# Kernel tuning notes

Hardware: AMD Instinct MI355X
Metric: run time of the kernel (lower is better)

Reference implementation:

```python
import jax, jax.numpy as jnp
import numpy as np

T = 33554432  # 2**25 timesteps
THRESHOLD = 0.5
DECAY = 0.01
LOWER_BOUND = 0.0
INTEGRATE_VALUE = "score"  # 'count' or 'score'


def setup_inputs() -> dict:
    key = jax.random.key(0)
    x = jax.random.normal(key, (T,), dtype=jnp.float32)
    return {"x": x}


def reference(x) -> jnp.ndarray:
    thr = jnp.asarray(THRESHOLD, dtype=x.dtype)
    decay = jnp.asarray(DECAY, dtype=x.dtype)
    lb = jnp.asarray(LOWER_BOUND, dtype=x.dtype)

    def step(score, data):
        inc = jnp.asarray(1.0, x.dtype) if INTEGRATE_VALUE == "count" else data
        accumulated = score + inc
        decayed = jnp.maximum(lb, score - decay)
        new_score = jnp.where(data >= thr, accumulated, decayed)
        return new_score, new_score

    _, out = jax.lax.scan(step, lb, x)
    return out
```

## Files before the change

kernel.cpp:

```cpp
#include <hip/hip_runtime.h>
#include <math.h>


#define BLOCK 256
#define PER_THREAD 16
#define CHUNK (BLOCK * PER_THREAD)
#define NGRID 7
#define NINF (-INFINITY)
#define BLOCKB 1024
#define PERB 8

typedef float f4 __attribute__((ext_vector_type(4)));

#define SWZ(s) ((s) ^ (((s) >> 3) & 7))

__device__ __forceinline__ void wave_incl_scan_fn(float& a, float& b, int lane) {
#pragma unroll
    for (int off = 1; off < 64; off <<= 1) {
        float pa = __shfl_up(a, off);
        float pb = __shfl_up(b, off);
        if (lane >= off) { b = fmaxf(pb + a, b); a = pa + a; }
    }
}

__global__ __launch_bounds__(BLOCK) void kA(const float* __restrict__ x,
                                            float* __restrict__ aggA,
                                            float* __restrict__ aggB,
                                            float* __restrict__ qarr,
                                            int n, int nb)
{
    __shared__ f4 stg[CHUNK / 4];
    __shared__ float red[4][2 + NGRID];

    const float gtab[NGRID]  = {0.015625f, 0.03125f, 0.0625f, 0.125f, 0.25f, 0.5f, 1.0f};
    const float igtab[NGRID] = {64.0f, 32.0f, 16.0f, 8.0f, 4.0f, 2.0f, 1.0f};

    int tid = threadIdx.x, lane = tid & 63, wave = tid >> 6;
    int b = blockIdx.x;
    bool fullblk = ((b + 1) * CHUNK <= n);

    float ta = 0.0f, tb = NINF;
    float q[NGRID];
#pragma unroll
    for (int k = 0; k < NGRID; ++k) q[k] = 0.0f;

    auto push = [&](float xv) {
        bool fire = (xv >= 0.5f);
        float a  = fire ? xv : -0.01f;
        float be = fire ? NINF : 0.0f;
        tb = fmaxf(tb + a, be);
        ta += a;
#pragma unroll
        for (int k = 0; k < NGRID; ++k)
            q[k] = fmaf(gtab[k], rintf(a * igtab[k]), q[k]);
    };

    if (fullblk) {
        const f4* xg = reinterpret_cast<const f4*>(x) + (size_t)b * (CHUNK / 4);
#pragma unroll
        for (int j = 0; j < 4; ++j) stg[SWZ(tid + 256 * j)] = xg[tid + 256 * j];
        __syncthreads();
#pragma unroll
        for (int jj = 0; jj < 4; ++jj) {
            f4 v = stg[SWZ(4 * tid + jj)];
            push(v.x); push(v.y); push(v.z); push(v.w);
        }
    } else {
        int base = b * CHUNK + tid * PER_THREAD;
        for (int j = 0; j < PER_THREAD; ++j) {
            int idx = base + j;
            if (idx < n) push(x[idx]);
        }
    }

    float ia = ta, ib = tb;
    wave_incl_scan_fn(ia, ib, lane);
    if (lane == 63) { red[wave][0] = ia; red[wave][1] = ib; }
#pragma unroll
    for (int k = 0; k < NGRID; ++k) {
        float v = q[k];
#pragma unroll
        for (int off = 32; off >= 1; off >>= 1) v += __shfl_down(v, off);
        if (lane == 0) red[wave][2 + k] = v;
    }
    __syncthreads();
    if (tid == 0) {
        float A = 0.0f, B = NINF;
#pragma unroll
        for (int w = 0; w < 4; ++w) {
            float wa = red[w][0], wb = red[w][1];
            B = fmaxf(B + wa, wb); A += wa;
        }
        aggA[b] = A; aggB[b] = B;
#pragma unroll
        for (int k = 0; k < NGRID; ++k)
            qarr[k * nb + b] = red[0][2+k] + red[1][2+k] + red[2][2+k] + red[3][2+k];
    }
}

__global__ __launch_bounds__(BLOCKB) void kB(const float* __restrict__ aggA,
                                             const float* __restrict__ aggB,
                                             const float* __restrict__ qarr,
                                             float* __restrict__ s_start, int nb)
{
    __shared__ float wt[16][2];
    int tid = threadIdx.x, lane = tid & 63, wv = tid >> 6;
    int start = tid * PERB;

    float Aj[PERB], Bj[PERB];
    bool inb = (start + PERB <= nb);
    if (inb) {
#pragma unroll
        for (int h = 0; h < PERB / 4; ++h) {
            f4 va = reinterpret_cast<const f4*>(aggA + start)[h];
            f4 vb = reinterpret_cast<const f4*>(aggB + start)[h];
            Aj[4*h+0] = va.x; Aj[4*h+1] = va.y; Aj[4*h+2] = va.z; Aj[4*h+3] = va.w;
            Bj[4*h+0] = vb.x; Bj[4*h+1] = vb.y; Bj[4*h+2] = vb.z; Bj[4*h+3] = vb.w;
        }
    } else {
#pragma unroll
        for (int j = 0; j < PERB; ++j) {
            int c = start + j;
            Aj[j] = (c < nb) ? aggA[c] : 0.0f;
            Bj[j] = (c < nb) ? aggB[c] : NINF;
        }
    }
    float ta = 0.0f, tb = NINF;
#pragma unroll
    for (int j = 0; j < PERB; ++j) { tb = fmaxf(tb + Aj[j], Bj[j]); ta += Aj[j]; }

    float ia = ta, ib = tb;
    wave_incl_scan_fn(ia, ib, lane);
    if (lane == 63) { wt[wv][0] = ia; wt[wv][1] = ib; }
    __syncthreads();
    float pa = 0.0f, pb = NINF;
    for (int w = 0; w < wv; ++w) {
        float wa = wt[w][0], wb = wt[w][1];
        pb = fmaxf(pb + wa, wb); pa += wa;
    }
    float xa = __shfl_up(ia, 1), xb = __shfl_up(ib, 1);
    if (lane == 0) { xa = 0.0f; xb = NINF; }
    float fa = pa + xa, fb = fmaxf(pb + xa, xb);
    __syncthreads();

    float selA[PERB], selB[PERB];
    float sE = fmaxf(fa, fb);
#pragma unroll
    for (int j = 0; j < PERB; ++j) {
        int c = start + j;
        bool v = (c < nb);
        float sA = Aj[j], sB = Bj[j];
        if (v && sE >= 131072.0f) {
            int E = (int)(__float_as_uint(sE) >> 23) - 127;
            int k = E - 17; if (k > NGRID - 1) k = NGRID - 1;
            sA = qarr[k * nb + c]; sB = NINF;
        }
        if (!v) { sA = 0.0f; sB = NINF; }
        selA[j] = sA; selB[j] = sB;
        sE = fmaxf(sE + Aj[j], Bj[j]);
    }

    float sta = 0.0f, stb = NINF;
#pragma unroll
    for (int j = 0; j < PERB; ++j) { stb = fmaxf(stb + selA[j], selB[j]); sta += selA[j]; }
    float ca = sta, cb = stb;
    wave_incl_scan_fn(ca, cb, lane);
    if (lane == 63) { wt[wv][0] = ca; wt[wv][1] = cb; }
    __syncthreads();
    float qa = 0.0f, qb = NINF;
    for (int w = 0; w < wv; ++w) {
        float wa = wt[w][0], wb = wt[w][1];
        qb = fmaxf(qb + wa, wb); qa += wa;
    }
    float ya = __shfl_up(ca, 1), yb = __shfl_up(cb, 1);
    if (lane == 0) { ya = 0.0f; yb = NINF; }
    float ga = qa + ya, gb = fmaxf(qb + ya, yb);

    float sS = fmaxf(ga, gb);
#pragma unroll
    for (int j = 0; j < PERB; ++j) {
        int c = start + j;
        if (c < nb) s_start[c] = sS;
        sS = fmaxf(sS + selA[j], selB[j]);
    }
}

__global__ __launch_bounds__(BLOCK) void kC(const float* __restrict__ x,
                                            const float* __restrict__ s_start,
                                            float* __restrict__ out, int n)
{
    __shared__ f4 stg[CHUNK / 4];
    __shared__ float wt[4][2];
    int tid = threadIdx.x, lane = tid & 63, wave = tid >> 6;
    int b = blockIdx.x;
    bool fullblk = ((b + 1) * CHUNK <= n);
    float s0c = s_start[b];

    float xs[PER_THREAD];
    float ta = 0.0f, tb = NINF;
    auto push = [&](float xv) {
        bool fire = (xv >= 0.5f);
        float a  = fire ? xv : -0.01f;
        float be = fire ? NINF : 0.0f;
        tb = fmaxf(tb + a, be);
        ta += a;
    };

    if (fullblk) {
        const f4* xg = reinterpret_cast<const f4*>(x) + (size_t)b * (CHUNK / 4);
#pragma unroll
        for (int j = 0; j < 4; ++j) stg[SWZ(tid + 256 * j)] = xg[tid + 256 * j];
        __syncthreads();
#pragma unroll
        for (int jj = 0; jj < 4; ++jj) {
            f4 v = stg[SWZ(4 * tid + jj)];
            xs[4*jj+0] = v.x; xs[4*jj+1] = v.y; xs[4*jj+2] = v.z; xs[4*jj+3] = v.w;
        }
#pragma unroll
        for (int j = 0; j < PER_THREAD; ++j) push(xs[j]);
    } else {
        int base = b * CHUNK + tid * PER_THREAD;
        for (int j = 0; j < PER_THREAD; ++j) {
            int idx = base + j;
            xs[j] = (idx < n) ? x[idx] : 0.0f;
            if (idx < n) push(xs[j]);
        }
    }

    float ia = ta, ib = tb;
    wave_incl_scan_fn(ia, ib, lane);
    if (lane == 63) { wt[wave][0] = ia; wt[wave][1] = ib; }
    __syncthreads();
    float xa = __shfl_up(ia, 1), xb = __shfl_up(ib, 1);
    if (lane == 0) { xa = 0.0f; xb = NINF; }
    float pa = 0.0f, pb = NINF;
    for (int w = 0; w < wave; ++w) {
        float wa = wt[w][0], wb = wt[w][1];
        pb = fmaxf(pb + wa, wb); pa += wa;
    }
    float exa = pa + xa, exb = fmaxf(pb + xa, xb);

    float s = fmaxf(s0c + exa, exb);

    if (fullblk) {
        float outs[PER_THREAD];
#pragma unroll
        for (int j = 0; j < PER_THREAD; ++j) {
            float xv = xs[j];
            float acc = s + xv;
            float dec = fmaxf(0.0f, s - 0.01f);
            s = (xv >= 0.5f) ? acc : dec;
            outs[j] = s;
        }
#pragma unroll
        for (int jj = 0; jj < 4; ++jj) {
            f4 o; o.x = outs[4*jj+0]; o.y = outs[4*jj+1]; o.z = outs[4*jj+2]; o.w = outs[4*jj+3];
            stg[SWZ(4 * tid + jj)] = o;
        }
        __syncthreads();
        f4* og = reinterpret_cast<f4*>(out) + (size_t)b * (CHUNK / 4);
#pragma unroll
        for (int j = 0; j < 4; ++j) og[tid + 256 * j] = stg[SWZ(tid + 256 * j)];
    } else {
        int base = b * CHUNK + tid * PER_THREAD;
        for (int j = 0; j < PER_THREAD; ++j) {
            int idx = base + j;
            if (idx < n) {
                float xv = xs[j];
                float acc = s + xv;
                float dec = fmaxf(0.0f, s - 0.01f);
                s = (xv >= 0.5f) ? acc : dec;
                out[idx] = s;
            }
        }
    }
}

extern "C" void kernel_launch(void* const* d_in, const int* in_sizes, int n_in,
                              void* d_out, int out_size, void* d_ws, size_t ws_size,
                              hipStream_t stream) {
    const float* x = (const float*)d_in[0];
    float* out = (float*)d_out;
    int n = in_sizes[0];
    int nb = (n + CHUNK - 1) / CHUNK;

    float* ws      = (float*)d_ws;
    float* aggA    = ws;
    float* aggB    = ws + nb;
    float* qarr    = ws + 2 * nb;
    float* s_start = ws + (2 + NGRID) * nb;

    kA<<<nb, BLOCK, 0, stream>>>(x, aggA, aggB, qarr, n, nb);
    kB<<<1, BLOCKB, 0, stream>>>(aggA, aggB, qarr, s_start, nb);
    kC<<<nb, BLOCK, 0, stream>>>(x, s_start, out, n);
}
```

Baseline: 84.21 us.

## Fold carry scan into output kernel using super-chunk aggregates

Removes the single-block middle kernel. The first pass now computes per-chunk and per-32K super-chunk aggregates, with each thread reading 128 contiguous elements directly and no LDS staging. Every output block then redundantly rescans the super-chunk aggregates in its prologue and walks up to 7 chunk carries to find its own start state. This saves one launch and one serialized tiny kernel, at the cost of redundant prologue work and scattered global reads in each of the 8192 output blocks. It also assumes nsc is at most 1024, because the 256 threads handle 4 super-chunks each.

```diff
diff --git a/kernel.cpp b/kernel.cpp
--- a/kernel.cpp
+++ b/kernel.cpp
@@ -4,14 +4,13 @@
 
 #define BLOCK 256
 #define PER_THREAD 16
-#define CHUNK (BLOCK * PER_THREAD)
+#define CHUNK 4096
+#define SUPER 32768
+#define PER_A 128
 #define NGRID 7
 #define NINF (-INFINITY)
-#define BLOCKB 1024
-#define PERB 8
 
 typedef float f4 __attribute__((ext_vector_type(4)));
-
 #define SWZ(s) ((s) ^ (((s) >> 3) & 7))
 
 __device__ __forceinline__ void wave_incl_scan_fn(float& a, float& b, int lane) {
@@ -23,21 +22,32 @@
     }
 }
 
+__device__ __forceinline__ void wave_seg32_scan_fn(float& a, float& b, int lane) {
+#pragma unroll
+    for (int off = 1; off < 32; off <<= 1) {
+        float pa = __shfl_up(a, off);
+        float pb = __shfl_up(b, off);
+        if ((lane & 31) >= off) { b = fmaxf(pb + a, b); a = pa + a; }
+    }
+}
+
 __global__ __launch_bounds__(BLOCK) void kA(const float* __restrict__ x,
-                                            float* __restrict__ aggA,
-                                            float* __restrict__ aggB,
-                                            float* __restrict__ qarr,
-                                            int n, int nb)
+                                            float* __restrict__ chunkA,
+                                            float* __restrict__ chunkB,
+                                            float* __restrict__ superA,
+                                            float* __restrict__ superB,
+                                            float* __restrict__ superQ,
+                                            int n, int nsc)
 {
-    __shared__ f4 stg[CHUNK / 4];
-    __shared__ float red[4][2 + NGRID];
+    __shared__ float red[4][NGRID];
+    __shared__ float cfn[8][2];
 
     const float gtab[NGRID]  = {0.015625f, 0.03125f, 0.0625f, 0.125f, 0.25f, 0.5f, 1.0f};
     const float igtab[NGRID] = {64.0f, 32.0f, 16.0f, 8.0f, 4.0f, 2.0f, 1.0f};
 
-    int tid = threadIdx.x, lane = tid & 63, wave = tid >> 6;
-    int b = blockIdx.x;
-    bool fullblk = ((b + 1) * CHUNK <= n);
+    int tid = threadIdx.x, lane = tid & 63, wv = tid >> 6;
+    int g = blockIdx.x;
+    size_t base = (size_t)g * SUPER + (size_t)tid * PER_A;
 
     float ta = 0.0f, tb = NINF;
     float q[NGRID];
@@ -55,147 +65,146 @@
             q[k] = fmaf(gtab[k], rintf(a * igtab[k]), q[k]);
     };
 
-    if (fullblk) {
-        const f4* xg = reinterpret_cast<const f4*>(x) + (size_t)b * (CHUNK / 4);
-#pragma unroll
-        for (int j = 0; j < 4; ++j) stg[SWZ(tid + 256 * j)] = xg[tid + 256 * j];
-        __syncthreads();
-#pragma unroll
-        for (int jj = 0; jj < 4; ++jj) {
-            f4 v = stg[SWZ(4 * tid + jj)];
+    if (base + PER_A <= (size_t)n) {
+        const f4* xg = reinterpret_cast<const f4*>(x + base);
+#pragma unroll
+        for (int j = 0; j < PER_A / 4; ++j) {
+            f4 v = xg[j];
             push(v.x); push(v.y); push(v.z); push(v.w);
         }
     } else {
-        int base = b * CHUNK + tid * PER_THREAD;
-        for (int j = 0; j < PER_THREAD; ++j) {
-            int idx = base + j;
-            if (idx < n) push(x[idx]);
+        for (int j = 0; j < PER_A; ++j) {
+            size_t idx = base + j;
+            if (idx < (size_t)n) push(x[idx]);
         }
     }
 
     float ia = ta, ib = tb;
-    wave_incl_scan_fn(ia, ib, lane);
-    if (lane == 63) { red[wave][0] = ia; red[wave][1] = ib; }
+    wave_seg32_scan_fn(ia, ib, lane);
+    if ((lane & 31) == 31) {
+        int ci = wv * 2 + (lane >> 5);
+        cfn[ci][0] = ia; cfn[ci][1] = ib;
+    }
 #pragma unroll
     for (int k = 0; k < NGRID; ++k) {
         float v = q[k];
 #pragma unroll
         for (int off = 32; off >= 1; off >>= 1) v += __shfl_down(v, off);
-        if (lane == 0) red[wave][2 + k] = v;
+        if (lane == 0) red[wv][k] = v;
     }
     __syncthreads();
     if (tid == 0) {
         float A = 0.0f, B = NINF;
 #pragma unroll
-        for (int w = 0; w < 4; ++w) {
-            float wa = red[w][0], wb = red[w][1];
-            B = fmaxf(B + wa, wb); A += wa;
-        }
-        aggA[b] = A; aggB[b] = B;
+        for (int i = 0; i < 8; ++i) { B = fmaxf(B + cfn[i][0], cfn[i][1]); A += cfn[i][0]; }
+        superA[g] = A; superB[g] = B;
 #pragma unroll
         for (int k = 0; k < NGRID; ++k)
-            qarr[k * nb + b] = red[0][2+k] + red[1][2+k] + red[2][2+k] + red[3][2+k];
-    }
-}
-
-__global__ __launch_bounds__(BLOCKB) void kB(const float* __restrict__ aggA,
-                                             const float* __restrict__ aggB,
-                                             const float* __restrict__ qarr,
-                                             float* __restrict__ s_start, int nb)
+            superQ[k * nsc + g] = red[0][k] + red[1][k] + red[2][k] + red[3][k];
+    }
+    if (tid < 8) { chunkA[g * 8 + tid] = cfn[tid][0]; chunkB[g * 8 + tid] = cfn[tid][1]; }
+}
+
+__global__ __launch_bounds__(BLOCK) void kC(const float* __restrict__ x,
+                                            const float* __restrict__ chunkA,
+                                            const float* __restrict__ chunkB,
+                                            const float* __restrict__ superA,
+                                            const float* __restrict__ superB,
+                                            const float* __restrict__ superQ,
+                                            float* __restrict__ out, int n, int nsc)
 {
-    __shared__ float wt[16][2];
+    __shared__ f4 stg[CHUNK / 4];
+    __shared__ float wt[4][2];
+    __shared__ float exS[BLOCK], slS[BLOCK];
+
     int tid = threadIdx.x, lane = tid & 63, wv = tid >> 6;
-    int start = tid * PERB;
-
-    float Aj[PERB], Bj[PERB];
-    bool inb = (start + PERB <= nb);
-    if (inb) {
-#pragma unroll
-        for (int h = 0; h < PERB / 4; ++h) {
-            f4 va = reinterpret_cast<const f4*>(aggA + start)[h];
-            f4 vb = reinterpret_cast<const f4*>(aggB + start)[h];
-            Aj[4*h+0] = va.x; Aj[4*h+1] = va.y; Aj[4*h+2] = va.z; Aj[4*h+3] = va.w;
-            Bj[4*h+0] = vb.x; Bj[4*h+1] = vb.y; Bj[4*h+2] = vb.z; Bj[4*h+3] = vb.w;
-        }
+    int blk = blockIdx.x;
+
+    int s0 = tid * 4;
+    float a_[4], b_[4];
+    if (s0 + 4 <= nsc) {
+        f4 va = reinterpret_cast<const f4*>(superA)[tid];
+        f4 vb = reinterpret_cast<const f4*>(superB)[tid];
+        a_[0] = va.x; a_[1] = va.y; a_[2] = va.z; a_[3] = va.w;
+        b_[0] = vb.x; b_[1] = vb.y; b_[2] = vb.z; b_[3] = vb.w;
     } else {
 #pragma unroll
-        for (int j = 0; j < PERB; ++j) {
-            int c = start + j;
-            Aj[j] = (c < nb) ? aggA[c] : 0.0f;
-            Bj[j] = (c < nb) ? aggB[c] : NINF;
-        }
-    }
-    float ta = 0.0f, tb = NINF;
-#pragma unroll
-    for (int j = 0; j < PERB; ++j) { tb = fmaxf(tb + Aj[j], Bj[j]); ta += Aj[j]; }
-
-    float ia = ta, ib = tb;
+        for (int i = 0; i < 4; ++i) {
+            int sc = s0 + i;
+            a_[i] = (sc < nsc) ? superA[sc] : 0.0f;
+            b_[i] = (sc < nsc) ? superB[sc] : NINF;
+        }
+    }
+    float ca = 0.0f, cb = NINF;
+#pragma unroll
+    for (int i = 0; i < 4; ++i) { cb = fmaxf(cb + a_[i], b_[i]); ca += a_[i]; }
+
+    float ia = ca, ib = cb;
     wave_incl_scan_fn(ia, ib, lane);
     if (lane == 63) { wt[wv][0] = ia; wt[wv][1] = ib; }
     __syncthreads();
+    float xa = __shfl_up(ia, 1), xb = __shfl_up(ib, 1);
+    if (lane == 0) { xa = 0.0f; xb = NINF; }
     float pa = 0.0f, pb = NINF;
     for (int w = 0; w < wv; ++w) {
         float wa = wt[w][0], wb = wt[w][1];
         pb = fmaxf(pb + wa, wb); pa += wa;
     }
-    float xa = __shfl_up(ia, 1), xb = __shfl_up(ib, 1);
-    if (lane == 0) { xa = 0.0f; xb = NINF; }
-    float fa = pa + xa, fb = fmaxf(pb + xa, xb);
-    __syncthreads();
-
-    float selA[PERB], selB[PERB];
-    float sE = fmaxf(fa, fb);
-#pragma unroll
-    for (int j = 0; j < PERB; ++j) {
-        int c = start + j;
-        bool v = (c < nb);
-        float sA = Aj[j], sB = Bj[j];
+    float ea = pa + xa, eb = fmaxf(pb + xa, xb);
+
+    float sE = fmaxf(ea, eb);
+    float sta = 0.0f, stb = NINF;
+#pragma unroll
+    for (int i = 0; i < 4; ++i) {
+        int sc = s0 + i;
+        bool v = (sc < nsc);
+        float sa = a_[i], sb = b_[i];
         if (v && sE >= 131072.0f) {
             int E = (int)(__float_as_uint(sE) >> 23) - 127;
             int k = E - 17; if (k > NGRID - 1) k = NGRID - 1;
-            sA = qarr[k * nb + c]; sB = NINF;
-        }
-        if (!v) { sA = 0.0f; sB = NINF; }
-        selA[j] = sA; selB[j] = sB;
-        sE = fmaxf(sE + Aj[j], Bj[j]);
-    }
-
-    float sta = 0.0f, stb = NINF;
-#pragma unroll
-    for (int j = 0; j < PERB; ++j) { stb = fmaxf(stb + selA[j], selB[j]); sta += selA[j]; }
-    float ca = sta, cb = stb;
-    wave_incl_scan_fn(ca, cb, lane);
-    if (lane == 63) { wt[wv][0] = ca; wt[wv][1] = cb; }
-    __syncthreads();
+            sa = superQ[k * nsc + sc]; sb = NINF;
+        }
+        if (!v) { sa = 0.0f; sb = NINF; }
+        stb = fmaxf(stb + sa, sb); sta += sa;
+        sE = fmaxf(sE + a_[i], b_[i]);
+    }
+
+    float ja = sta, jb = stb;
+    wave_incl_scan_fn(ja, jb, lane);
+    __syncthreads();
+    if (lane == 63) { wt[wv][0] = ja; wt[wv][1] = jb; }
+    __syncthreads();
+    float ya = __shfl_up(ja, 1), yb = __shfl_up(jb, 1);
+    if (lane == 0) { ya = 0.0f; yb = NINF; }
     float qa = 0.0f, qb = NINF;
     for (int w = 0; w < wv; ++w) {
         float wa = wt[w][0], wb = wt[w][1];
         qb = fmaxf(qb + wa, wb); qa += wa;
     }
-    float ya = __shfl_up(ca, 1), yb = __shfl_up(cb, 1);
-    if (lane == 0) { ya = 0.0f; yb = NINF; }
     float ga = qa + ya, gb = fmaxf(qb + ya, yb);
 
-    float sS = fmaxf(ga, gb);
-#pragma unroll
-    for (int j = 0; j < PERB; ++j) {
-        int c = start + j;
-        if (c < nb) s_start[c] = sS;
-        sS = fmaxf(sS + selA[j], selB[j]);
-    }
-}
-
-__global__ __launch_bounds__(BLOCK) void kC(const float* __restrict__ x,
-                                            const float* __restrict__ s_start,
-                                            float* __restrict__ out, int n)
-{
-    __shared__ f4 stg[CHUNK / 4];
-    __shared__ float wt[4][2];
-    int tid = threadIdx.x, lane = tid & 63, wave = tid >> 6;
-    int b = blockIdx.x;
-    bool fullblk = ((b + 1) * CHUNK <= n);
-    float s0c = s_start[b];
-
+    exS[tid] = fmaxf(ea, eb);
+    slS[tid] = fmaxf(ga, gb);
+    __syncthreads();
+
+    int sc0 = blk >> 3, j0 = sc0 >> 2;
+    float sE2 = exS[j0], sS2 = slS[j0];
+    for (int c = 4 * j0; c < sc0; ++c) {
+        float a = superA[c], b = superB[c];
+        float sa = a, sb = b;
+        if (sE2 >= 131072.0f) {
+            int E = (int)(__float_as_uint(sE2) >> 23) - 127;
+            int k = E - 17; if (k > NGRID - 1) k = NGRID - 1;
+            sa = superQ[k * nsc + c]; sb = NINF;
+        }
+        sS2 = fmaxf(sS2 + sa, sb); sE2 = fmaxf(sE2 + a, b);
+    }
+    float s0c = sS2;
+    for (int c = (sc0 << 3); c < blk; ++c)
+        s0c = fmaxf(s0c + chunkA[c], chunkB[c]);
+    __syncthreads();
+
+    bool fullblk = ((size_t)(blk + 1) * CHUNK <= (size_t)n);
     float xs[PER_THREAD];
     float ta = 0.0f, tb = NINF;
     auto push = [&](float xv) {
@@ -207,7 +216,7 @@
     };
 
     if (fullblk) {
-        const f4* xg = reinterpret_cast<const f4*>(x) + (size_t)b * (CHUNK / 4);
+        const f4* xg = reinterpret_cast<const f4*>(x) + (size_t)blk * (CHUNK / 4);
 #pragma unroll
         for (int j = 0; j < 4; ++j) stg[SWZ(tid + 256 * j)] = xg[tid + 256 * j];
         __syncthreads();
@@ -219,26 +228,26 @@
 #pragma unroll
         for (int j = 0; j < PER_THREAD; ++j) push(xs[j]);
     } else {
-        int base = b * CHUNK + tid * PER_THREAD;
+        size_t base = (size_t)blk * CHUNK + (size_t)tid * PER_THREAD;
         for (int j = 0; j < PER_THREAD; ++j) {
-            int idx = base + j;
-            xs[j] = (idx < n) ? x[idx] : 0.0f;
-            if (idx < n) push(xs[j]);
-        }
-    }
-
-    float ia = ta, ib = tb;
-    wave_incl_scan_fn(ia, ib, lane);
-    if (lane == 63) { wt[wave][0] = ia; wt[wave][1] = ib; }
-    __syncthreads();
-    float xa = __shfl_up(ia, 1), xb = __shfl_up(ib, 1);
-    if (lane == 0) { xa = 0.0f; xb = NINF; }
-    float pa = 0.0f, pb = NINF;
-    for (int w = 0; w < wave; ++w) {
+            size_t idx = base + j;
+            xs[j] = (idx < (size_t)n) ? x[idx] : 0.0f;
+            if (idx < (size_t)n) push(xs[j]);
+        }
+    }
+
+    float ia2 = ta, ib2 = tb;
+    wave_incl_scan_fn(ia2, ib2, lane);
+    if (lane == 63) { wt[wv][0] = ia2; wt[wv][1] = ib2; }
+    __syncthreads();
+    float xa2 = __shfl_up(ia2, 1), xb2 = __shfl_up(ib2, 1);
+    if (lane == 0) { xa2 = 0.0f; xb2 = NINF; }
+    float pa2 = 0.0f, pb2 = NINF;
+    for (int w = 0; w < wv; ++w) {
         float wa = wt[w][0], wb = wt[w][1];
-        pb = fmaxf(pb + wa, wb); pa += wa;
-    }
-    float exa = pa + xa, exb = fmaxf(pb + xa, xb);
+        pb2 = fmaxf(pb2 + wa, wb); pa2 += wa;
+    }
+    float exa = pa2 + xa2, exb = fmaxf(pb2 + xa2, xb2);
 
     float s = fmaxf(s0c + exa, exb);
 
@@ -252,20 +261,21 @@
             s = (xv >= 0.5f) ? acc : dec;
             outs[j] = s;
         }
+        __syncthreads();
 #pragma unroll
         for (int jj = 0; jj < 4; ++jj) {
             f4 o; o.x = outs[4*jj+0]; o.y = outs[4*jj+1]; o.z = outs[4*jj+2]; o.w = outs[4*jj+3];
             stg[SWZ(4 * tid + jj)] = o;
         }
         __syncthreads();
-        f4* og = reinterpret_cast<f4*>(out) + (size_t)b * (CHUNK / 4);
+        f4* og = reinterpret_cast<f4*>(out) + (size_t)blk * (CHUNK / 4);
 #pragma unroll
         for (int j = 0; j < 4; ++j) og[tid + 256 * j] = stg[SWZ(tid + 256 * j)];
     } else {
-        int base = b * CHUNK + tid * PER_THREAD;
+        size_t base = (size_t)blk * CHUNK + (size_t)tid * PER_THREAD;
         for (int j = 0; j < PER_THREAD; ++j) {
-            int idx = base + j;
-            if (idx < n) {
+            size_t idx = base + j;
+            if (idx < (size_t)n) {
                 float xv = xs[j];
                 float acc = s + xv;
                 float dec = fmaxf(0.0f, s - 0.01f);
@@ -282,15 +292,16 @@
     const float* x = (const float*)d_in[0];
     float* out = (float*)d_out;
     int n = in_sizes[0];
-    int nb = (n + CHUNK - 1) / CHUNK;
-
-    float* ws      = (float*)d_ws;
-    float* aggA    = ws;
-    float* aggB    = ws + nb;
-    float* qarr    = ws + 2 * nb;
-    float* s_start = ws + (2 + NGRID) * nb;
-
-    kA<<<nb, BLOCK, 0, stream>>>(x, aggA, aggB, qarr, n, nb);
-    kB<<<1, BLOCKB, 0, stream>>>(aggA, aggB, qarr, s_start, nb);
-    kC<<<nb, BLOCK, 0, stream>>>(x, s_start, out, n);
-}
+    int nb  = (n + CHUNK - 1) / CHUNK;
+    int nsc = (n + SUPER - 1) / SUPER;
+
+    float* ws     = (float*)d_ws;
+    float* chunkA = ws;
+    float* chunkB = ws + nb;
+    float* superA = ws + 2 * nb;
+    float* superB = superA + nsc;
+    float* superQ = superB + nsc;
+
+    kA<<<nsc, BLOCK, 0, stream>>>(x, chunkA, chunkB, superA, superB, superQ, n, nsc);
+    kC<<<nb, BLOCK, 0, stream>>>(x, chunkA, chunkB, superA, superB, superQ, out, n, nsc);
+}
```

Measured after the change: 83.47 us. No clear change (-0.9%).
